# Kernel optimization log

Measured on AMD Instinct MI355X. Metric: run time of the kernel, lower is better.

## Reference

```python
import jax, jax.numpy as jnp
import numpy as np

H = 16      # heads
DH = 64     # dim_head
EPS = 1e-6
ROPE_BASE = 10000.0


def _rms_norm(t, w):
    # torch.nn.RMSNorm over last dim (inner_dim)
    var = jnp.mean(t * t, axis=-1, keepdims=True)
    return t * jax.lax.rsqrt(var + EPS) * w


def _rope(t):
    # t: (b, n, h, d) with d split as (d/2, 2) interleaved pairs
    b, n, h, d = t.shape
    theta = 1.0 / (ROPE_BASE ** (jnp.arange(0, d, 2, dtype=jnp.float32) / d))  # (d/2,)
    pos_theta = jnp.arange(n, dtype=jnp.float32)[:, None] * theta[None, :]     # (n, d/2)
    cos = jnp.cos(pos_theta)[None, :, None, :]  # (1, n, 1, d/2)
    sin = jnp.sin(pos_theta)[None, :, None, :]
    tp = t.reshape(b, n, h, d // 2, 2)
    x0, x1 = tp[..., 0], tp[..., 1]
    r0 = cos * x0 - sin * x1
    r1 = sin * x0 + cos * x1
    return jnp.stack([r0, r1], axis=-1).reshape(b, n, h, d)


def setup_inputs() -> dict:
    key = jax.random.key(0)
    ks = jax.random.split(key, 5)
    B, N, D = 2, 2048, 1024
    inner = H * DH
    scale = 1.0 / np.sqrt(D)
    return {
        "x": jax.random.normal(ks[0], (B, N, D), dtype=jnp.float32),
        "Wq": jax.random.normal(ks[1], (D, inner), dtype=jnp.float32) * scale,
        "Wkv": jax.random.normal(ks[2], (D, 2 * inner), dtype=jnp.float32) * scale,
        "norm_q_w": jnp.ones((inner,), dtype=jnp.float32),
        "norm_k_w": jnp.ones((inner,), dtype=jnp.float32),
        "Wo": jax.random.normal(ks[3], (inner, D), dtype=jnp.float32) * scale,
        "bo": jnp.zeros((D,), dtype=jnp.float32),
    }


def reference(x, Wq, Wkv, norm_q_w, norm_k_w, Wo, bo):
    B, N, D = x.shape
    q = x @ Wq                       # (b, n, inner)
    kv = x @ Wkv                     # (b, n, 2*inner)
    k, v = jnp.split(kv, 2, axis=-1)
    q = _rms_norm(q, norm_q_w)
    k = _rms_norm(k, norm_k_w)
    # (b, n, h, d)
    q = q.reshape(B, N, H, DH)
    k = k.reshape(B, N, H, DH)
    v = v.reshape(B, N, H, DH)
    q = _rope(q)
    k = _rope(k)
    # SDPA: softmax(q k^T / sqrt(d)) v, heads as batch dim
    scores = jnp.einsum("bnhd,bmhd->bhnm", q, k) / np.sqrt(DH)
    attn = jax.nn.softmax(scores, axis=-1)
    out = jnp.einsum("bhnm,bmhd->bnhd", attn, v).reshape(B, N, H * DH)
    return out @ Wo + bo
```

## Files before the change

### kernel.cpp

```cpp
#include <hip/hip_runtime.h>

typedef __bf16 bf16;
typedef _Float16 f16;
typedef __bf16 bf16x8 __attribute__((ext_vector_type(8)));
typedef _Float16 f16x4 __attribute__((ext_vector_type(4)));
typedef _Float16 f16x8 __attribute__((ext_vector_type(8)));
typedef float f32x4 __attribute__((ext_vector_type(4)));
typedef float f32x16 __attribute__((ext_vector_type(16)));

__device__ __forceinline__ void async16(const void* g, void* l) {
  __builtin_amdgcn_global_load_lds(
      (const __attribute__((address_space(1))) unsigned int*)g,
      (__attribute__((address_space(3))) unsigned int*)l, 16, 0, 0);
}

__device__ __forceinline__ unsigned cvtpk(float a, float b) {
  unsigned r;
  asm("v_cvt_pk_bf16_f32 %0, %1, %2" : "=v"(r) : "v"(a), "v"(b));
  return r;
}

__device__ __forceinline__ void swap32(unsigned& a, unsigned& b) {
  asm("v_permlane32_swap_b32 %0, %1" : "+v"(a), "+v"(b));
}

__global__ __launch_bounds__(256) void castx(const float* __restrict__ in,
                                             f16* __restrict__ out) {
  long i = ((long)blockIdx.x * 256 + threadIdx.x) * 4;
  f32x4 v = *(const f32x4*)(in + i);
  f16x4 o;
#pragma unroll
  for (int j = 0; j < 4; j++) o[j] = (f16)v[j];
  *(f16x4*)(out + i) = o;
}

__global__ __launch_bounds__(256) void tcast(const float* __restrict__ in,
                                             f16* __restrict__ out, int R, int C) {
  __shared__ float tile[32][33];
  int tx = threadIdx.x, ty = threadIdx.y;
  int c = blockIdx.x * 32 + tx;
#pragma unroll
  for (int i = 0; i < 4; i++) {
    int r = blockIdx.y * 32 + ty + i * 8;
    tile[ty + i * 8][tx] = in[(long)r * C + c];
  }
  __syncthreads();
  int c2 = blockIdx.y * 32 + tx;
#pragma unroll
  for (int i = 0; i < 4; i++) {
    int r2 = blockIdx.x * 32 + ty + i * 8;
    out[(long)r2 * R + c2] = (f16)tile[tx][ty + i * 8];
  }
}

__global__ __launch_bounds__(256) void vtrans(const f16* __restrict__ src,
                                              bf16* __restrict__ vtf) {
  __shared__ f16 tile[32][33];
  int tx = threadIdx.x, ty = threadIdx.y;
  int n0 = blockIdx.x * 32, d0 = blockIdx.y * 32, bh = blockIdx.z;
  int b = bh >> 4, h = bh & 15;
#pragma unroll
  for (int i = 0; i < 4; i++) {
    int n = n0 + ty + i * 8;
    tile[ty + i * 8][tx] = src[(long)(b * 2048 + n) * 3072 + h * 64 + d0 + tx];
  }
  __syncthreads();
#pragma unroll
  for (int i = 0; i < 4; i++) {
    int d = d0 + ty + i * 8;
    int n = n0 + tx;
    long off = ((((long)bh * 32 + (n >> 6)) * 8 + (d >> 5) * 4 + ((n & 63) >> 4)) * 64 +
                ((n >> 3) & 1) * 32 + (d & 31)) * 8 + (n & 7);
    vtf[off] = (bf16)(float)tile[tx][ty + i * 8];
  }
}

template <int MODE>
__global__ __launch_bounds__(512) void gemm_f16(const f16* __restrict__ A_g,
                                                const f16* __restrict__ B_g,
                                                float* __restrict__ p0,
                                                float* __restrict__ p1,
                                                f16* __restrict__ outh,
                                                int M, int N, int K) {
  __shared__ __align__(16) f16 AL[2][4096], BL[2][4096];
  int t = threadIdx.x, lane = t & 63, w = t >> 6;
  int wm = w >> 1, wn = w & 1;
  int m0 = blockIdx.y * 128, n0 = blockIdx.x * 128;
  int fm = lane & 15, fq = lane >> 4;
  int kseg = K / gridDim.z;
  int kstart = blockIdx.z * kseg;
  int nk = kseg / 32;

  const f16* ap = A_g + (long)(m0 + w * 16 + fm) * K + kstart + fq * 8;
  const f16* bp = B_g + (long)(n0 + w * 16 + fm) * K + kstart + fq * 8;

  f32x4 acc[2][4];
#pragma unroll
  for (int i = 0; i < 2; i++)
#pragma unroll
    for (int j = 0; j < 4; j++) acc[i][j] = f32x4{0.f, 0.f, 0.f, 0.f};

  async16(ap, &AL[0][w * 512]);
  async16(bp, &BL[0][w * 512]);

  for (int it = 0; it < nk; it++) {
    int cur = it & 1;
    __syncthreads();
    if (it < nk - 1) {
      int ko = (it + 1) * 32;
      async16(ap + ko, &AL[cur ^ 1][w * 512]);
      async16(bp + ko, &BL[cur ^ 1][w * 512]);
    }
    f16x8 a[2], bfr[4];
#pragma unroll
    for (int i = 0; i < 2; i++)
      a[i] = *(const f16x8*)&AL[cur][(wm * 2 + i) * 512 + lane * 8];
#pragma unroll
    for (int j = 0; j < 4; j++)
      bfr[j] = *(const f16x8*)&BL[cur][(wn * 4 + j) * 512 + lane * 8];
#pragma unroll
    for (int i = 0; i < 2; i++)
#pragma unroll
      for (int j = 0; j < 4; j++)
        acc[i][j] = __builtin_amdgcn_mfma_f32_16x16x32_f16(a[i], bfr[j], acc[i][j], 0, 0, 0);
  }

  float* dst = blockIdx.z ? p1 : p0;
#pragma unroll
  for (int i = 0; i < 2; i++)
#pragma unroll
    for (int j = 0; j < 4; j++) {
      int c = n0 + (wn * 4 + j) * 16 + fm;
#pragma unroll
      for (int e = 0; e < 4; e++) {
        int r = m0 + (wm * 2 + i) * 16 + fq * 4 + e;
        if (MODE == 0)
          dst[(long)r * N + c] = acc[i][j][e];
        else
          outh[(long)r * N + c] = (f16)acc[i][j][e];
      }
    }
}

__global__ __launch_bounds__(256) void addbias(const float* __restrict__ p0,
                                               const float* __restrict__ p1,
                                               const float* __restrict__ bias,
                                               float* __restrict__ out) {
  long i = ((long)blockIdx.x * 256 + threadIdx.x) * 4;
  f32x4 a = *(const f32x4*)(p0 + i);
  f32x4 b = *(const f32x4*)(p1 + i);
  f32x4 c = *(const f32x4*)(bias + (i & 1023));
  *(f32x4*)(out + i) = a + b + c;
}

__global__ __launch_bounds__(256) void normrope(const f16* __restrict__ src,
                                                const float* __restrict__ wqn,
                                                const float* __restrict__ wkn,
                                                f16* __restrict__ qf,
                                                f16* __restrict__ kff) {
  int row = blockIdx.x, which = blockIdx.y;
  const f16* sp = src + (long)row * 3072 + which * 1024;
  const float* w = which ? wkn : wqn;
  float scale = which ? 1.0f : 0.125f;
  int t = threadIdx.x;
  int j0 = t * 4;

  f16x4 xh = *(const f16x4*)(sp + j0);
  float xv[4];
#pragma unroll
  for (int j = 0; j < 4; j++) xv[j] = (float)xh[j];
  float ss = xv[0] * xv[0] + xv[1] * xv[1] + xv[2] * xv[2] + xv[3] * xv[3];
#pragma unroll
  for (int off = 32; off > 0; off >>= 1) ss += __shfl_down(ss, off);
  __shared__ float red[4];
  if ((t & 63) == 0) red[t >> 6] = ss;
  __syncthreads();
  float total = red[0] + red[1] + red[2] + red[3];
  float nsc = rsqrtf(total * (1.0f / 1024.0f) + 1e-6f) * scale;

  int n = row & 2047;
  f16x4 o;
#pragma unroll
  for (int pp = 0; pp < 2; pp++) {
    int j = j0 + 2 * pp;
    int ii = (j & 63) >> 1;
    float theta = __expf((float)ii * (-9.210340371976184f / 32.0f));
    float ang = (float)n * theta;
    float sn, cs;
    __sincosf(ang, &sn, &cs);
    float a0 = xv[2 * pp] * nsc * w[j];
    float a1 = xv[2 * pp + 1] * nsc * w[j + 1];
    o[2 * pp] = (f16)(cs * a0 - sn * a1);
    o[2 * pp + 1] = (f16)(sn * a0 + cs * a1);
  }
  if (which == 0) {
    *(f16x4*)(qf + (long)row * 1024 + j0) = o;
  } else {
    int b2 = row >> 11;
    int h2 = j0 >> 6, dl = j0 & 63;
    long off = ((((long)(b2 * 16 + h2) * 32 + (n >> 6)) * 8 + ((n >> 5) & 1) * 4 +
                 (dl >> 4)) * 64 + ((dl >> 3) & 1) * 32 + (n & 31)) * 8 + (dl & 7);
    *(f16x4*)(kff + off) = o;
  }
}

__global__ __launch_bounds__(256) void attn_mfma(const f16* __restrict__ qf,
                                                 const f16* __restrict__ kff,
                                                 const bf16* __restrict__ vtf,
                                                 f16* __restrict__ pO,
                                                 float* __restrict__ pl) {
  __shared__ __align__(16) f16 KhL[2][4096];
  __shared__ __align__(16) bf16 VtL[2][4096];

  int t = threadIdx.x;
  int lane = t & 63, w = t >> 6;
  int lo5 = lane & 31, hi = lane >> 5;
  int z = blockIdx.z;
  int b = z >> 1, ksp = z & 1;
  int h = blockIdx.y, q0 = blockIdx.x * 128;

  const f16* qb = qf + ((long)(b * 2048 + q0 + w * 32 + lo5)) * 1024 + h * 64 + hi * 8;
  f16x8 qfr[4];
#pragma unroll
  for (int ks = 0; ks < 4; ks++) qfr[ks] = *(const f16x8*)(qb + ks * 16);

  const f16* kg = kff + ((long)(b * 16 + h)) * 131072 + (2 * w) * 512 + lane * 8;
  const bf16* vg = vtf + ((long)(b * 16 + h)) * 131072 + (2 * w) * 512 + lane * 8;

  f32x16 Ot[2];
#pragma unroll
  for (int i = 0; i < 16; i++) {
    Ot[0][i] = 0.f;
    Ot[1][i] = 0.f;
  }
  float l_ = 0.f;

  int kb0 = ksp * 16;

#define STAGE(buf, kb)                                                     \
  {                                                                        \
    async16(kg + (long)(kb) * 4096, (char*)KhL[buf] + (2 * w) * 1024);     \
    async16(kg + (long)(kb) * 4096 + 512,                                  \
            (char*)KhL[buf] + (2 * w + 1) * 1024);                         \
    async16(vg + (long)(kb) * 4096, (char*)VtL[buf] + (2 * w) * 1024);     \
    async16(vg + (long)(kb) * 4096 + 512,                                  \
            (char*)VtL[buf] + (2 * w + 1) * 1024);                         \
  }

  STAGE(0, kb0);

  for (int it = 0; it < 16; it++) {
    int cur = it & 1;
    __syncthreads();
    if (it < 15) STAGE(cur ^ 1, kb0 + it + 1);

    const char* kbase = (const char*)KhL[cur];
    const char* vbase = (const char*)VtL[cur];

    f32x16 s0, s1;
#pragma unroll
    for (int i = 0; i < 16; i++) {
      s0[i] = 0.f;
      s1[i] = 0.f;
    }
#pragma unroll
    for (int ks = 0; ks < 4; ks++) {
      f16x8 k0 = *(const f16x8*)(kbase + ks * 1024 + (long)lane * 16);
      f16x8 k1 = *(const f16x8*)(kbase + (4 + ks) * 1024 + (long)lane * 16);
      s0 = __builtin_amdgcn_mfma_f32_32x32x16_f16(k0, qfr[ks], s0, 0, 0, 0);
      s1 = __builtin_amdgcn_mfma_f32_32x32x16_f16(k1, qfr[ks], s1, 0, 0, 0);
    }

    union PF {
      unsigned u[4];
      bf16x8 v;
    } pf[4];
#pragma unroll
    for (int nt = 0; nt < 2; nt++) {
      f32x16 s = nt ? s1 : s0;
      float pv[16];
#pragma unroll
      for (int r = 0; r < 16; r++) {
        pv[r] = __expf(s[r]);
        l_ += pv[r];
      }
#pragma unroll
      for (int g = 0; g < 2; g++) {
        unsigned c01 = cvtpk(pv[g * 8 + 0], pv[g * 8 + 1]);
        unsigned c23 = cvtpk(pv[g * 8 + 2], pv[g * 8 + 3]);
        unsigned c45 = cvtpk(pv[g * 8 + 4], pv[g * 8 + 5]);
        unsigned c67 = cvtpk(pv[g * 8 + 6], pv[g * 8 + 7]);
        swap32(c01, c45);
        swap32(c23, c67);
        pf[nt * 2 + g].u[0] = c01;
        pf[nt * 2 + g].u[1] = c23;
        pf[nt * 2 + g].u[2] = c45;
        pf[nt * 2 + g].u[3] = c67;
      }
    }

#pragma unroll
    for (int ks = 0; ks < 4; ks++) {
      bf16x8 v0 = *(const bf16x8*)(vbase + ks * 1024 + (long)lane * 16);
      bf16x8 v1 = *(const bf16x8*)(vbase + (4 + ks) * 1024 + (long)lane * 16);
      Ot[0] = __builtin_amdgcn_mfma_f32_32x32x16_bf16(v0, pf[ks].v, Ot[0], 0, 0, 0);
      Ot[1] = __builtin_amdgcn_mfma_f32_32x32x16_bf16(v1, pf[ks].v, Ot[1], 0, 0, 0);
    }
  }
#undef STAGE

  l_ += __shfl_xor(l_, 32);
  float inv = 1.0f / l_;

  long rowi = ((long)((ksp * 2 + b) * 16 + h)) * 2048 + q0 + w * 32 + lo5;
  f16* op = pO + rowi * 64;
#pragma unroll
  for (int dt = 0; dt < 2; dt++)
#pragma unroll
    for (int g4 = 0; g4 < 4; g4++) {
      f16x4 o4;
#pragma unroll
      for (int e = 0; e < 4; e++) o4[e] = (f16)(Ot[dt][g4 * 4 + e] * inv);
      *(f16x4*)(op + dt * 32 + g4 * 8 + hi * 4) = o4;
    }
  if (hi == 0) pl[rowi] = l_;
}

__global__ __launch_bounds__(256) void attn_combine(const f16* __restrict__ pO,
                                                    const float* __restrict__ pl,
                                                    f16* __restrict__ af) {
  int dg = threadIdx.x & 15;
  int qi = threadIdx.x >> 4;
  int q = blockIdx.x * 16 + qi;
  int h = blockIdx.y, b = blockIdx.z;
  long r0 = ((long)(b * 16 + h)) * 2048 + q;
  long r1 = ((long)((2 + b) * 16 + h)) * 2048 + q;
  float l0 = pl[r0], l1 = pl[r1];
  float w0 = l0 / (l0 + l1), w1 = 1.0f - w0;
  f16x4 a = *(const f16x4*)(pO + r0 * 64 + dg * 4);
  f16x4 c = *(const f16x4*)(pO + r1 * 64 + dg * 4);
  f16x4 o;
#pragma unroll
  for (int e = 0; e < 4; e++) o[e] = (f16)((float)a[e] * w0 + (float)c[e] * w1);
  *(f16x4*)(af + ((long)(b * 2048 + q)) * 1024 + h * 64 + dg * 4) = o;
}

extern "C" void kernel_launch(void* const* d_in, const int* in_sizes, int n_in,
                              void* d_out, int out_size, void* d_ws, size_t ws_size,
                              hipStream_t stream) {
  const float* x = (const float*)d_in[0];
  const float* Wq = (const float*)d_in[1];
  const float* Wkv = (const float*)d_in[2];
  const float* nqw = (const float*)d_in[3];
  const float* nkw = (const float*)d_in[4];
  const float* Wo = (const float*)d_in[5];
  const float* bo = (const float*)d_in[6];
  float* out = (float*)d_out;

  char* ws = (char*)d_ws;
  const long MB = 1l << 20;
  f16* xf     = (f16*)(ws);
  f16* Wqkv_t = (f16*)(ws + 8 * MB);
  f16* qkv_f  = (f16*)(ws + 14 * MB);
  f16* qfb    = (f16*)(ws + 38 * MB);
  f16* kffb   = (f16*)(ws + 46 * MB);
  bf16* vtfb  = (bf16*)(ws + 54 * MB);
  f16* pOb    = (f16*)(ws + 14 * MB);
  float* plb  = (float*)(ws + 30 * MB);
  f16* afb    = (f16*)(ws);
  f16* Wo_t   = (f16*)(ws + 8 * MB);
  float* p0   = (float*)(ws + 14 * MB);
  float* p1   = (float*)(ws + 30 * MB);

  dim3 tb(32, 8);
  castx<<<4096, 256, 0, stream>>>(x, xf);
  tcast<<<dim3(32, 32), tb, 0, stream>>>(Wq, Wqkv_t, 1024, 1024);
  tcast<<<dim3(64, 32), tb, 0, stream>>>(Wkv, Wqkv_t + 1024l * 1024, 1024, 2048);

  gemm_f16<1><<<dim3(24, 32), 512, 0, stream>>>(xf, Wqkv_t, nullptr, nullptr,
                                                qkv_f, 4096, 3072, 1024);

  normrope<<<dim3(4096, 2), 256, 0, stream>>>(qkv_f, nqw, nkw, qfb, kffb);

  vtrans<<<dim3(64, 2, 32), tb, 0, stream>>>(qkv_f + 2048, vtfb);

  attn_mfma<<<dim3(16, 16, 4), 256, 0, stream>>>(qfb, kffb, vtfb, pOb, plb);

  attn_combine<<<dim3(128, 16, 2), 256, 0, stream>>>(pOb, plb, afb);

  tcast<<<dim3(32, 32), tb, 0, stream>>>(Wo, Wo_t, 1024, 1024);

  gemm_f16<0><<<dim3(8, 32, 2), 512, 0, stream>>>(afb, Wo_t, p0, p1, nullptr,
                                                  4096, 1024, 1024);

  addbias<<<4096, 256, 0, stream>>>(p0, p1, bo, out);
}
```

Baseline: 252.4 us.

## Triple-buffer attention K/V staging with vmcnt waits, exp2 softmax and MFMA priority

Moves the attention inner loop from double to triple buffering of K/V tiles in LDS. Each step waits with an explicit vmcnt count plus a raw barrier, so the next two tiles stay in flight while the current one is computed. It also folds log2(e) into the Q scale so a raw v_exp_f32 replaces __expf, and wraps the MFMA chains in s_setprio so matrix work is favoured across waves. This costs more LDS and relies on hand-written waitcnt ordering being correct.

```diff
diff --git a/kernel.cpp b/kernel.cpp
--- a/kernel.cpp
+++ b/kernel.cpp
@@ -22,6 +22,12 @@
 
 __device__ __forceinline__ void swap32(unsigned& a, unsigned& b) {
   asm("v_permlane32_swap_b32 %0, %1" : "+v"(a), "+v"(b));
+}
+
+__device__ __forceinline__ float exp2i(float x) {
+  float r;
+  asm("v_exp_f32 %0, %1" : "=v"(r) : "v"(x));
+  return r;
 }
 
 __global__ __launch_bounds__(256) void castx(const float* __restrict__ in,
@@ -161,7 +167,7 @@
   int row = blockIdx.x, which = blockIdx.y;
   const f16* sp = src + (long)row * 3072 + which * 1024;
   const float* w = which ? wkn : wqn;
-  float scale = which ? 1.0f : 0.125f;
+  float scale = which ? 1.0f : 0.18033688011112042f;
   int t = threadIdx.x;
   int j0 = t * 4;
 
@@ -204,13 +210,62 @@
   }
 }
 
+__device__ __forceinline__ void attn_tile(const char* kbase, const char* vbase,
+                                          const f16x8* qfr, const f32x16& Z,
+                                          f32x16* Ot, float& l_, int la) {
+  union PF {
+    unsigned u[4];
+    bf16x8 v;
+  } pf[4];
+#pragma unroll
+  for (int nt = 0; nt < 2; nt++) {
+    f16x8 k0 = *(const f16x8*)(kbase + (nt * 4 + 0) * 1024 + la);
+    f16x8 k1 = *(const f16x8*)(kbase + (nt * 4 + 1) * 1024 + la);
+    f16x8 k2 = *(const f16x8*)(kbase + (nt * 4 + 2) * 1024 + la);
+    f16x8 k3 = *(const f16x8*)(kbase + (nt * 4 + 3) * 1024 + la);
+    __builtin_amdgcn_s_setprio(1);
+    f32x16 s = __builtin_amdgcn_mfma_f32_32x32x16_f16(k0, qfr[0], Z, 0, 0, 0);
+    s = __builtin_amdgcn_mfma_f32_32x32x16_f16(k1, qfr[1], s, 0, 0, 0);
+    s = __builtin_amdgcn_mfma_f32_32x32x16_f16(k2, qfr[2], s, 0, 0, 0);
+    s = __builtin_amdgcn_mfma_f32_32x32x16_f16(k3, qfr[3], s, 0, 0, 0);
+    __builtin_amdgcn_s_setprio(0);
+    float pv[16];
+#pragma unroll
+    for (int r = 0; r < 16; r++) {
+      pv[r] = exp2i(s[r]);
+      l_ += pv[r];
+    }
+#pragma unroll
+    for (int g = 0; g < 2; g++) {
+      unsigned c01 = cvtpk(pv[g * 8 + 0], pv[g * 8 + 1]);
+      unsigned c23 = cvtpk(pv[g * 8 + 2], pv[g * 8 + 3]);
+      unsigned c45 = cvtpk(pv[g * 8 + 4], pv[g * 8 + 5]);
+      unsigned c67 = cvtpk(pv[g * 8 + 6], pv[g * 8 + 7]);
+      swap32(c01, c45);
+      swap32(c23, c67);
+      pf[nt * 2 + g].u[0] = c01;
+      pf[nt * 2 + g].u[1] = c23;
+      pf[nt * 2 + g].u[2] = c45;
+      pf[nt * 2 + g].u[3] = c67;
+    }
+  }
+  __builtin_amdgcn_s_setprio(1);
+#pragma unroll
+  for (int ks = 0; ks < 4; ks++) {
+    bf16x8 v0 = *(const bf16x8*)(vbase + ks * 1024 + la);
+    bf16x8 v1 = *(const bf16x8*)(vbase + (4 + ks) * 1024 + la);
+    Ot[0] = __builtin_amdgcn_mfma_f32_32x32x16_bf16(v0, pf[ks].v, Ot[0], 0, 0, 0);
+    Ot[1] = __builtin_amdgcn_mfma_f32_32x32x16_bf16(v1, pf[ks].v, Ot[1], 0, 0, 0);
+  }
+  __builtin_amdgcn_s_setprio(0);
+}
+
 __global__ __launch_bounds__(256) void attn_mfma(const f16* __restrict__ qf,
                                                  const f16* __restrict__ kff,
                                                  const bf16* __restrict__ vtf,
                                                  f16* __restrict__ pO,
                                                  float* __restrict__ pl) {
-  __shared__ __align__(16) f16 KhL[2][4096];
-  __shared__ __align__(16) bf16 VtL[2][4096];
+  __shared__ __align__(16) char smem[49152];
 
   int t = threadIdx.x;
   int lane = t & 63, w = t >> 6;
@@ -218,6 +273,7 @@
   int z = blockIdx.z;
   int b = z >> 1, ksp = z & 1;
   int h = blockIdx.y, q0 = blockIdx.x * 128;
+  int la = lane * 16;
 
   const f16* qb = qf + ((long)(b * 2048 + q0 + w * 32 + lo5)) * 1024 + h * 64 + hi * 8;
   f16x8 qfr[4];
@@ -233,80 +289,45 @@
     Ot[0][i] = 0.f;
     Ot[1][i] = 0.f;
   }
+  f32x16 Z;
+#pragma unroll
+  for (int i = 0; i < 16; i++) Z[i] = 0.f;
   float l_ = 0.f;
 
   int kb0 = ksp * 16;
 
-#define STAGE(buf, kb)                                                     \
-  {                                                                        \
-    async16(kg + (long)(kb) * 4096, (char*)KhL[buf] + (2 * w) * 1024);     \
-    async16(kg + (long)(kb) * 4096 + 512,                                  \
-            (char*)KhL[buf] + (2 * w + 1) * 1024);                         \
-    async16(vg + (long)(kb) * 4096, (char*)VtL[buf] + (2 * w) * 1024);     \
-    async16(vg + (long)(kb) * 4096 + 512,                                  \
-            (char*)VtL[buf] + (2 * w + 1) * 1024);                         \
+#define STAGE(buf, kb)                                                        \
+  {                                                                           \
+    async16(kg + (long)(kb) * 4096, smem + (buf) * 8192 + (2 * w) * 1024);    \
+    async16(kg + (long)(kb) * 4096 + 512,                                     \
+            smem + (buf) * 8192 + (2 * w + 1) * 1024);                        \
+    async16(vg + (long)(kb) * 4096,                                           \
+            smem + 24576 + (buf) * 8192 + (2 * w) * 1024);                    \
+    async16(vg + (long)(kb) * 4096 + 512,                                     \
+            smem + 24576 + (buf) * 8192 + (2 * w + 1) * 1024);                \
   }
 
   STAGE(0, kb0);
-
-  for (int it = 0; it < 16; it++) {
-    int cur = it & 1;
-    __syncthreads();
-    if (it < 15) STAGE(cur ^ 1, kb0 + it + 1);
-
-    const char* kbase = (const char*)KhL[cur];
-    const char* vbase = (const char*)VtL[cur];
-
-    f32x16 s0, s1;
-#pragma unroll
-    for (int i = 0; i < 16; i++) {
-      s0[i] = 0.f;
-      s1[i] = 0.f;
-    }
-#pragma unroll
-    for (int ks = 0; ks < 4; ks++) {
-      f16x8 k0 = *(const f16x8*)(kbase + ks * 1024 + (long)lane * 16);
-      f16x8 k1 = *(const f16x8*)(kbase + (4 + ks) * 1024 + (long)lane * 16);
-      s0 = __builtin_amdgcn_mfma_f32_32x32x16_f16(k0, qfr[ks], s0, 0, 0, 0);
-      s1 = __builtin_amdgcn_mfma_f32_32x32x16_f16(k1, qfr[ks], s1, 0, 0, 0);
-    }
-
-    union PF {
-      unsigned u[4];
-      bf16x8 v;
-    } pf[4];
-#pragma unroll
-    for (int nt = 0; nt < 2; nt++) {
-      f32x16 s = nt ? s1 : s0;
-      float pv[16];
-#pragma unroll
-      for (int r = 0; r < 16; r++) {
-        pv[r] = __expf(s[r]);
-        l_ += pv[r];
-      }
-#pragma unroll
-      for (int g = 0; g < 2; g++) {
-        unsigned c01 = cvtpk(pv[g * 8 + 0], pv[g * 8 + 1]);
-        unsigned c23 = cvtpk(pv[g * 8 + 2], pv[g * 8 + 3]);
-        unsigned c45 = cvtpk(pv[g * 8 + 4], pv[g * 8 + 5]);
-        unsigned c67 = cvtpk(pv[g * 8 + 6], pv[g * 8 + 7]);
-        swap32(c01, c45);
-        swap32(c23, c67);
-        pf[nt * 2 + g].u[0] = c01;
-        pf[nt * 2 + g].u[1] = c23;
-        pf[nt * 2 + g].u[2] = c45;
-        pf[nt * 2 + g].u[3] = c67;
-      }
-    }
-
-#pragma unroll
-    for (int ks = 0; ks < 4; ks++) {
-      bf16x8 v0 = *(const bf16x8*)(vbase + ks * 1024 + (long)lane * 16);
-      bf16x8 v1 = *(const bf16x8*)(vbase + (4 + ks) * 1024 + (long)lane * 16);
-      Ot[0] = __builtin_amdgcn_mfma_f32_32x32x16_bf16(v0, pf[ks].v, Ot[0], 0, 0, 0);
-      Ot[1] = __builtin_amdgcn_mfma_f32_32x32x16_bf16(v1, pf[ks].v, Ot[1], 0, 0, 0);
-    }
-  }
+  STAGE(1, kb0 + 1);
+
+  int cur = 0;
+  for (int it = 0; it < 15; it++) {
+    asm volatile("s_waitcnt vmcnt(4)" ::: "memory");
+    __builtin_amdgcn_s_barrier();
+    asm volatile("" ::: "memory");
+    if (it < 14) {
+      int nb = cur + 2;
+      if (nb >= 3) nb -= 3;
+      STAGE(nb, kb0 + it + 2);
+    }
+    attn_tile(smem + cur * 8192, smem + 24576 + cur * 8192, qfr, Z, Ot, l_, la);
+    cur++;
+    if (cur == 3) cur = 0;
+  }
+  asm volatile("s_waitcnt vmcnt(0)" ::: "memory");
+  __builtin_amdgcn_s_barrier();
+  asm volatile("" ::: "memory");
+  attn_tile(smem + cur * 8192, smem + 24576 + cur * 8192, qfr, Z, Ot, l_, la);
 #undef STAGE
 
   l_ += __shfl_xor(l_, 32);
```

After: 252.1 us. About the same (-0.1%).
